# Optimization experiments

Measured on AMD Instinct MI355X. Metric: run time of the kernel, lower is better.

Reference implementation:

```python
import jax, jax.numpy as jnp
import numpy as np

BETA = 1.0 / np.sqrt(768.0).astype(np.float32)


def setup_inputs() -> dict:
    key = jax.random.key(0)
    k1, k2, k3 = jax.random.split(key, 3)
    x = jax.random.normal(k1, (32, 512, 768), dtype=jnp.float32)
    # torch nn.Linear(dim, n_prototype).weight has shape [n_prototype, dim]
    w_lookup = jax.random.normal(k2, (4096, 768), dtype=jnp.float32) * 0.02
    # torch nn.Linear(n_prototype, dim).weight has shape [dim, n_prototype]
    w_content = jax.random.normal(k3, (768, 4096), dtype=jnp.float32) * 0.02
    return {"x": x, "w_lookup": w_lookup, "w_content": w_content}


def reference(x, w_lookup, w_content):
    # scores: [b, s, n_prototype] = x @ w_lookup^T, scaled by 1/sqrt(dim)
    scores = jnp.einsum("bsd,pd->bsp", x, w_lookup) * jnp.asarray(BETA, x.dtype)
    lookup = jax.nn.softmax(scores, axis=-1)
    # content: [b, s, dim] = lookup @ w_content^T
    content = jnp.einsum("bsp,dp->bsd", lookup, w_content)
    return content  # dropout is identity in eval / p=0.0
```

## Files before the change

kernel.cpp:

```cpp
#include <hip/hip_runtime.h>
#include <hip/hip_bf16.h>


#define NTOK   16384
#define DIM    768
#define NPROT  4096
#define BETA_F 0.03608439182428583f

typedef __bf16 bf16_t;
typedef __bf16 bf16x8 __attribute__((ext_vector_type(8)));
typedef float  floatx4 __attribute__((ext_vector_type(4)));

__device__ __forceinline__ void async_copy16(const bf16_t* g, void* l) {
  __builtin_amdgcn_global_load_lds(
      (__attribute__((address_space(1))) const void*)g,
      (__attribute__((address_space(3))) void*)l, 16, 0, 0);
}

__global__ __launch_bounds__(256) void cvt_all(
    const float* __restrict__ x, const float* __restrict__ wl,
    const float* __restrict__ wc, bf16_t* __restrict__ xb,
    bf16_t* __restrict__ wlb, bf16_t* __restrict__ wcb,
    int nx8, int nw8, int nc8) {
  int i = blockIdx.x * 256 + threadIdx.x;
  const float* in; bf16_t* out; int k; int dv;
  if (i < nx8) {
    in = x; out = xb; k = i;
    const int m = k / 96, kv = k % 96;
    const int kt = kv >> 3, kr = kv & 7;
    const int sf = (((m >> 4) & 15) << 1) + (kr >> 2);
    const int l  = (m & 15) + ((kr & 3) << 4);
    dv = (((m >> 8) * 12 + kt) * 32 + sf) * 64 + l;
  } else if (i < nx8 + nw8) {
    in = wl; out = wlb; k = i - nx8;
    const int p = k / 96, kv = k % 96;
    const int kt = kv >> 3, kr = kv & 7;
    const int sf = (((p >> 4) & 15) << 1) + (kr >> 2);
    const int l  = (p & 15) + ((kr & 3) << 4);
    dv = (((p >> 8) * 12 + kt) * 32 + sf) * 64 + l;
  } else if (i < nx8 + nw8 + nc8) {
    in = wc; out = wcb; k = i - nx8 - nw8;
    const int d = k / 512, pv = k % 512;
    const int kt = pv >> 3, kr = pv & 7;
    const int dd = d % 192;
    const int sf = ((dd >> 4) << 1) + (kr >> 2);
    const int l  = (dd & 15) + ((kr & 3) << 4);
    dv = (((d / 192) * 64 + kt) * 24 + sf) * 64 + l;
  } else return;
  const float4* in4 = (const float4*)in;
  float4 a = in4[2 * k], b = in4[2 * k + 1];
  bf16x8 o;
  o[0] = (bf16_t)a.x; o[1] = (bf16_t)a.y; o[2] = (bf16_t)a.z; o[3] = (bf16_t)a.w;
  o[4] = (bf16_t)b.x; o[5] = (bf16_t)b.y; o[6] = (bf16_t)b.z; o[7] = (bf16_t)b.w;
  ((bf16x8*)out)[dv] = o;
}

__global__ __launch_bounds__(512, 2)
void gemm256(const bf16_t* __restrict__ A, const bf16_t* __restrict__ B,
             bf16_t* __restrict__ P, float* __restrict__ rowsum,
             const int K, const int N, const int nN) {
  __shared__ char lds[131072];

  const int tid = threadIdx.x;
  const int l   = tid & 63;
  const int w   = tid >> 6;
  const int wr  = w >> 2;
  const int wc  = w & 3;
  const int lr  = l & 15;

  const int nwg   = gridDim.x;
  const int chunk = nwg >> 3;
  const int wg    = (blockIdx.x & 7) * chunk + (blockIdx.x >> 3);
  const int m0    = (wg / nN) * 256;
  const int n0    = (wg % nN) * 256;

  const int T = K >> 6;
  const int abase = (m0 >> 8) * T * 16384 + l * 8;
  const int bbase = (n0 >> 8) * T * 16384 + l * 8;
  int asf[2][2], bsf[2][2];
#pragma unroll
  for (int h = 0; h < 2; ++h)
#pragma unroll
    for (int j = 0; j < 2; ++j) {
      const int s = j * 8 + w;
      asf[h][j] = ((h * 8 + (s >> 1)) * 2 + (s & 1)) * 512;
      bsf[h][j] = asf[h][j];
    }

  auto stageA = [&](int slot, int kt, int h) {
#pragma unroll
    for (int j = 0; j < 2; ++j) {
      const int s  = j * 8 + w;
      const int sf = (h * 8 + (s >> 1)) * 2 + (s & 1);
      async_copy16(A + abase + kt * 16384 + asf[h][j],
                   lds + slot * 65536 + sf * 1024);
    }
  };
  auto stageB = [&](int slot, int kt, int h) {
#pragma unroll
    for (int j = 0; j < 2; ++j) {
      const int s  = j * 8 + w;
      const int sf = (h * 8 + (s >> 1)) * 2 + (s & 1);
      async_copy16(B + bbase + kt * 16384 + bsf[h][j],
                   lds + slot * 65536 + 32768 + sf * 1024);
    }
  };

  bf16x8 af[4][2], bg[4][2];
  auto loadA = [&](int slot, int mh) {
#pragma unroll
    for (int q = 0; q < 4; ++q)
#pragma unroll
      for (int ks = 0; ks < 2; ++ks)
        af[q][ks] = *(const bf16x8*)(lds + slot * 65536 +
                        ((mh * 8 + q * 2 + wr) * 2 + ks) * 1024 + l * 16);
  };
  auto loadB = [&](int slot, int nh, int qb) {
#pragma unroll
    for (int q = 0; q < 2; ++q)
#pragma unroll
      for (int ks = 0; ks < 2; ++ks)
        bg[qb + q][ks] = *(const bf16x8*)(lds + slot * 65536 + 32768 +
                        ((nh * 8 + q * 4 + wc) * 2 + ks) * 1024 + l * 16);
  };

  const floatx4 z = {0.f, 0.f, 0.f, 0.f};
  floatx4 acc[8][4];
#pragma unroll
  for (int mt = 0; mt < 8; ++mt)
#pragma unroll
    for (int nt = 0; nt < 4; ++nt) acc[mt][nt] = z;

  auto mma = [&](int mq, int nq) {
    __builtin_amdgcn_s_setprio(1);
#pragma unroll
    for (int q = 0; q < 4; ++q)
#pragma unroll
      for (int r = 0; r < 2; ++r)
#pragma unroll
        for (int ks = 0; ks < 2; ++ks)
          acc[mq * 4 + q][nq * 2 + r] = __builtin_amdgcn_mfma_f32_16x16x32_bf16(
              af[q][ks], bg[nq * 2 + r][ks], acc[mq * 4 + q][nq * 2 + r], 0, 0, 0);
    __builtin_amdgcn_s_setprio(0);
  };

#define BAR()    __builtin_amdgcn_s_barrier()
#define LGKM0()  asm volatile("s_waitcnt lgkmcnt(0)")
#define LGKM8()  asm volatile("s_waitcnt lgkmcnt(8)")
#define VM(n)    asm volatile("s_waitcnt vmcnt(" #n ")" ::: "memory")

  stageA(0, 0, 0); stageB(0, 0, 0); stageB(0, 0, 1); stageA(0, 0, 1);
  stageA(1, 1, 0); stageB(1, 1, 0); stageB(1, 1, 1);
  VM(6);
  BAR();

#pragma unroll 1
  for (int t = 0; t < T - 2; t += 2) {
    loadA(0, 0); loadB(0, 0, 0);
    stageA(1, t + 1, 1);
    LGKM8();
    BAR(); LGKM0(); mma(0, 0); BAR();
    loadB(0, 1, 2);
    stageA(0, t + 2, 0);
    BAR(); LGKM0(); mma(0, 1); BAR();
    loadA(0, 1);
    stageB(0, t + 2, 0);
    BAR(); LGKM0(); mma(1, 1); BAR();
    stageB(0, t + 2, 1);
    BAR(); mma(1, 0); VM(6); BAR();
    loadA(1, 0); loadB(1, 0, 0);
    stageA(0, t + 2, 1);
    LGKM8();
    BAR(); LGKM0(); mma(0, 0); BAR();
    loadB(1, 1, 2);
    stageA(1, t + 3, 0);
    BAR(); LGKM0(); mma(0, 1); BAR();
    loadA(1, 1);
    stageB(1, t + 3, 0);
    BAR(); LGKM0(); mma(1, 1); BAR();
    stageB(1, t + 3, 1);
    BAR(); mma(1, 0); VM(6); BAR();
  }

  loadA(0, 0); loadB(0, 0, 0);
  stageA(1, T - 1, 1);
  LGKM8();
  BAR(); LGKM0(); mma(0, 0); BAR();
  loadB(0, 1, 2);
  BAR(); LGKM0(); mma(0, 1); BAR();
  loadA(0, 1);
  BAR(); LGKM0(); mma(1, 1); BAR();
  BAR(); mma(1, 0); VM(0); BAR();
  loadA(1, 0); loadB(1, 0, 0);
  BAR(); LGKM0(); mma(0, 0); BAR();
  loadB(1, 1, 2);
  BAR(); LGKM0(); mma(0, 1); BAR();
  loadA(1, 1);
  BAR(); LGKM0(); mma(1, 1); BAR();
  mma(1, 0);

  const int hi4 = (l >> 4) << 2;
#pragma unroll
  for (int mt = 0; mt < 8; ++mt) {
    const int row = m0 + (mt * 2 + wr) * 16 + hi4;
    float rs[4] = {0.f, 0.f, 0.f, 0.f};
#pragma unroll
    for (int nt = 0; nt < 4; ++nt) {
      const int col = n0 + (nt * 4 + wc) * 16 + lr;
#pragma unroll
      for (int i = 0; i < 4; ++i) {
        const float e = __expf(acc[mt][nt][i] * BETA_F);
        P[(row + i) * N + col] = (bf16_t)e;
        rs[i] += e;
      }
    }
#pragma unroll
    for (int i = 0; i < 4; ++i) {
      float s = rs[i];
      s += __shfl_xor(s, 1);
      s += __shfl_xor(s, 2);
      s += __shfl_xor(s, 4);
      s += __shfl_xor(s, 8);
      if (lr == 0) atomicAdd(&rowsum[row + i], s);
    }
  }
}

__global__ __launch_bounds__(512, 2)
void gemm192(const bf16_t* __restrict__ A, const bf16_t* __restrict__ B,
             float* __restrict__ O, const float* __restrict__ rowsum,
             const int K, const int N) {
  __shared__ char lds[114688];

  const int tid = threadIdx.x;
  const int l   = tid & 63;
  const int w   = tid >> 6;
  const int wr  = w >> 2;
  const int wc  = w & 3;
  const int lr  = l & 15;
  const int lk  = (l >> 4) << 3;

  const int wg = (blockIdx.x & 7) * 32 + (blockIdx.x >> 3);
  const int m0 = (wg >> 2) * 256;
  const int n0 = (wg & 3) * 192;

  int aoff[2][2];
#pragma unroll
  for (int h = 0; h < 2; ++h)
#pragma unroll
    for (int j = 0; j < 2; ++j) {
      const int s     = j * 8 + w;
      const int mfrag = h * 8 + (s >> 1);
      const int ks    = s & 1;
      aoff[h][j] = (m0 + mfrag * 16 + lr) * K + ks * 32 + lk;
    }
  const int bb = (n0 / 192) * 64 * 12288 + l * 8;
  int bsf[3];
#pragma unroll
  for (int t = 0; t < 3; ++t) bsf[t] = (t * 8 + w) * 512;

  auto stageA = [&](int slot, int kt, int h) {
#pragma unroll
    for (int j = 0; j < 2; ++j) {
      const int s  = j * 8 + w;
      const int sf = (h * 8 + (s >> 1)) * 2 + (s & 1);
      async_copy16(A + aoff[h][j] + kt * 64, lds + slot * 57344 + sf * 1024);
    }
  };
  auto stageBt = [&](int slot, int kt, int t) {
    async_copy16(B + bb + kt * 12288 + bsf[t],
                 lds + slot * 57344 + 32768 + (t * 8 + w) * 1024 + l * 16);
  };

  bf16x8 af[4][2], bg[3][2];
  auto loadA = [&](int slot, int mh) {
#pragma unroll
    for (int q = 0; q < 4; ++q)
#pragma unroll
      for (int ks = 0; ks < 2; ++ks)
        af[q][ks] = *(const bf16x8*)(lds + slot * 57344 +
                        ((mh * 8 + q * 2 + wr) * 2 + ks) * 1024 + l * 16);
  };
  auto loadBn = [&](int slot, int nlo, int ncnt) {
    for (int r = 0; r < ncnt; ++r)
#pragma unroll
      for (int ks = 0; ks < 2; ++ks)
        bg[nlo + r][ks] = *(const bf16x8*)(lds + slot * 57344 + 32768 +
                        (((wc * 3 + nlo + r) * 2 + ks) << 10) + l * 16);
  };

  const floatx4 z = {0.f, 0.f, 0.f, 0.f};
  floatx4 acc[8][3];
#pragma unroll
  for (int mt = 0; mt < 8; ++mt)
#pragma unroll
    for (int nt = 0; nt < 3; ++nt) acc[mt][nt] = z;

  auto mma = [&](int mq, int nlo, int ncnt) {
    __builtin_amdgcn_s_setprio(1);
#pragma unroll
    for (int q = 0; q < 4; ++q)
      for (int r = 0; r < ncnt; ++r)
#pragma unroll
        for (int ks = 0; ks < 2; ++ks)
          acc[mq * 4 + q][nlo + r] = __builtin_amdgcn_mfma_f32_16x16x32_bf16(
              af[q][ks], bg[nlo + r][ks], acc[mq * 4 + q][nlo + r], 0, 0, 0);
    __builtin_amdgcn_s_setprio(0);
  };

  const int T = K >> 6;

  stageA(0, 0, 0); stageA(0, 0, 1);
  stageBt(0, 0, 0); stageBt(0, 0, 1); stageBt(0, 0, 2);
  stageA(1, 1, 0);
  stageBt(1, 1, 0); stageBt(1, 1, 1); stageBt(1, 1, 2);
  VM(5);
  BAR();

#pragma unroll 1
  for (int t = 0; t < T - 2; t += 2) {
#pragma unroll
    for (int u = 0; u < 2; ++u) {
      const int p = u;
      loadA(p, 0); loadBn(p, 0, 2);
      stageA(p ^ 1, t + u + 1, 1);
      LGKM8();
      BAR(); LGKM0(); mma(0, 0, 2); BAR();
      loadBn(p, 2, 1);
      stageA(p, t + u + 2, 0);
      BAR(); LGKM0(); mma(0, 2, 1); BAR();
      loadA(p, 1);
      stageBt(p, t + u + 2, 0); stageBt(p, t + u + 2, 1);
      BAR(); LGKM0(); mma(1, 0, 2); BAR();
      stageBt(p, t + u + 2, 2);
      BAR(); mma(1, 2, 1); VM(5); BAR();
    }
  }

  loadA(0, 0); loadBn(0, 0, 2);
  stageA(1, T - 1, 1);
  LGKM8();
  BAR(); LGKM0(); mma(0, 0, 2); BAR();
  loadBn(0, 2, 1);
  BAR(); LGKM0(); mma(0, 2, 1); BAR();
  loadA(0, 1);
  BAR(); LGKM0(); mma(1, 0, 2); BAR();
  BAR(); mma(1, 2, 1); VM(0); BAR();
  loadA(1, 0); loadBn(1, 0, 2);
  BAR(); LGKM0(); mma(0, 0, 2); BAR();
  loadBn(1, 2, 1);
  BAR(); LGKM0(); mma(0, 2, 1); BAR();
  loadA(1, 1);
  BAR(); LGKM0(); mma(1, 0, 2); BAR();
  mma(1, 2, 1);

#undef BAR
#undef LGKM0
#undef LGKM8
#undef VM

  const int hi4 = (l >> 4) << 2;
#pragma unroll
  for (int mt = 0; mt < 8; ++mt) {
    const int row = m0 + (mt * 2 + wr) * 16 + hi4;
#pragma unroll
    for (int i = 0; i < 4; ++i) {
      const float inv = 1.0f / rowsum[row + i];
#pragma unroll
      for (int nt = 0; nt < 3; ++nt)
        O[(row + i) * N + n0 + (wc * 3 + nt) * 16 + lr] = acc[mt][nt][i] * inv;
    }
  }
}

__global__ __launch_bounds__(256) void hopfield_fallback(
    const float* __restrict__ x, const float* __restrict__ wl,
    const float* __restrict__ wc, float* __restrict__ out) {
  __shared__ float  xs[8 * 768];
  __shared__ bf16_t ps[8 * 4096];
  __shared__ float  rs[8];
  const int tid = threadIdx.x;
  const int r0  = blockIdx.x * 8;
  if (tid < 8) rs[tid] = 0.f;
  for (int i = tid; i < 8 * 768; i += 256)
    xs[i] = x[(r0 + (i / 768)) * 768 + (i % 768)];
  __syncthreads();

  float lsum[8] = {0, 0, 0, 0, 0, 0, 0, 0};
  for (int p = tid; p < 4096; p += 256) {
    float s[8] = {0, 0, 0, 0, 0, 0, 0, 0};
    for (int d = 0; d < 768; ++d) {
      const float wv = wl[p * 768 + d];
#pragma unroll
      for (int r = 0; r < 8; ++r) s[r] += xs[r * 768 + d] * wv;
    }
#pragma unroll
    for (int r = 0; r < 8; ++r) {
      const float e = __expf(s[r] * BETA_F);
      ps[r * 4096 + p] = (bf16_t)e;
      lsum[r] += e;
    }
  }
#pragma unroll
  for (int r = 0; r < 8; ++r) atomicAdd(&rs[r], lsum[r]);
  __syncthreads();

  for (int d = tid; d < 768; d += 256) {
    float o[8] = {0, 0, 0, 0, 0, 0, 0, 0};
    for (int p = 0; p < 4096; ++p) {
      const float wv = wc[d * 4096 + p];
#pragma unroll
      for (int r = 0; r < 8; ++r) o[r] += (float)ps[r * 4096 + p] * wv;
    }
#pragma unroll
    for (int r = 0; r < 8; ++r) out[(r0 + r) * 768 + d] = o[r] / rs[r];
  }
}

extern "C" void kernel_launch(void* const* d_in, const int* in_sizes, int n_in,
                              void* d_out, int out_size, void* d_ws, size_t ws_size,
                              hipStream_t stream) {
  (void)in_sizes; (void)n_in; (void)out_size;
  const float* x  = (const float*)d_in[0];
  const float* wl = (const float*)d_in[1];
  const float* wc = (const float*)d_in[2];
  float* out = (float*)d_out;

  const size_t xb_e = (size_t)NTOK * DIM;
  const size_t wl_e = (size_t)NPROT * DIM;
  const size_t wc_e = (size_t)DIM * NPROT;
  const size_t P_e  = (size_t)NTOK * NPROT;
  const size_t need = (xb_e + wl_e + wc_e + P_e) * 2 + (size_t)NTOK * 4;

  if (ws_size >= need) {
    char* ws = (char*)d_ws;
    bf16_t* xb  = (bf16_t*)ws;  ws += xb_e * 2;
    bf16_t* wlb = (bf16_t*)ws;  ws += wl_e * 2;
    bf16_t* wcb = (bf16_t*)ws;  ws += wc_e * 2;
    bf16_t* P   = (bf16_t*)ws;  ws += P_e * 2;
    float* rowsum = (float*)ws;

    hipMemsetAsync(rowsum, 0, NTOK * sizeof(float), stream);
    const int nx8 = (int)(xb_e / 8), nw8 = (int)(wl_e / 8), nc8 = (int)(wc_e / 8);
    cvt_all<<<(nx8 + nw8 + nc8 + 255) / 256, 256, 0, stream>>>(
        x, wl, wc, xb, wlb, wcb, nx8, nw8, nc8);
    gemm256<<<dim3((NTOK / 256) * (NPROT / 256)), 512, 0, stream>>>(
        xb, wlb, P, rowsum, DIM, NPROT, NPROT / 256);
    gemm192<<<dim3(256), 512, 0, stream>>>(
        P, wcb, out, rowsum, NPROT, DIM);
  } else {
    hopfield_fallback<<<NTOK / 8, 256, 0, stream>>>(x, wl, wc, out);
  }
}
```

Baseline: 385.8 us.

## Write softmax numerators in pre-tiled fragment layout for the second GEMM

The first GEMM's epilogue now stores exp(scores) into P in the same blocked 64-wide k-tile/fragment layout that the A operand staging uses. The second GEMM then loads A with contiguous 1KB fragment copies instead of strided row-major addressing. The aim is more coalesced, contiguous async global-to-LDS loads in the second GEMM. The cost is scattered 2-byte stores in the first kernel's epilogue and some macro redefinition shuffling.

```diff
diff --git a/kernel.cpp b/kernel.cpp
--- a/kernel.cpp
+++ b/kernel.cpp
@@ -77,14 +77,13 @@
   const int T = K >> 6;
   const int abase = (m0 >> 8) * T * 16384 + l * 8;
   const int bbase = (n0 >> 8) * T * 16384 + l * 8;
-  int asf[2][2], bsf[2][2];
+  int asf[2][2];
 #pragma unroll
   for (int h = 0; h < 2; ++h)
 #pragma unroll
     for (int j = 0; j < 2; ++j) {
       const int s = j * 8 + w;
       asf[h][j] = ((h * 8 + (s >> 1)) * 2 + (s & 1)) * 512;
-      bsf[h][j] = asf[h][j];
     }
 
   auto stageA = [&](int slot, int kt, int h) {
@@ -101,7 +100,7 @@
     for (int j = 0; j < 2; ++j) {
       const int s  = j * 8 + w;
       const int sf = (h * 8 + (s >> 1)) * 2 + (s & 1);
-      async_copy16(B + bbase + kt * 16384 + bsf[h][j],
+      async_copy16(B + bbase + kt * 16384 + asf[h][j],
                    lds + slot * 65536 + 32768 + sf * 1024);
     }
   };
@@ -199,18 +198,30 @@
   BAR(); LGKM0(); mma(1, 1); BAR();
   mma(1, 0);
 
+#undef BAR
+#undef LGKM0
+#undef LGKM8
+#undef VM
+
   const int hi4 = (l >> 4) << 2;
+  const int pband = (m0 >> 8) * 64;
 #pragma unroll
   for (int mt = 0; mt < 8; ++mt) {
-    const int row = m0 + (mt * 2 + wr) * 16 + hi4;
+    const int mfrag = mt * 2 + wr;
+    const int rowb  = m0 + mfrag * 16 + hi4;
     float rs[4] = {0.f, 0.f, 0.f, 0.f};
 #pragma unroll
     for (int nt = 0; nt < 4; ++nt) {
-      const int col = n0 + (nt * 4 + wc) * 16 + lr;
+      const int nn   = nt * 4 + wc;
+      const int kt   = (n0 >> 6) + (nn >> 2);
+      const int sf   = mfrag * 2 + ((nn >> 1) & 1);
+      const int ksel = ((nn & 1) << 1) + (lr >> 3);
+      bf16_t* dst = P + ((size_t)((pband + kt) * 32 + sf) * 512 +
+                         (hi4 + (ksel << 4)) * 8 + (lr & 7));
 #pragma unroll
       for (int i = 0; i < 4; ++i) {
         const float e = __expf(acc[mt][nt][i] * BETA_F);
-        P[(row + i) * N + col] = (bf16_t)e;
+        dst[i * 8] = (bf16_t)e;
         rs[i] += e;
       }
     }
@@ -221,7 +232,7 @@
       s += __shfl_xor(s, 2);
       s += __shfl_xor(s, 4);
       s += __shfl_xor(s, 8);
-      if (lr == 0) atomicAdd(&rowsum[row + i], s);
+      if (lr == 0) atomicAdd(&rowsum[rowb + i], s);
     }
   }
 }
@@ -238,21 +249,19 @@
   const int wr  = w >> 2;
   const int wc  = w & 3;
   const int lr  = l & 15;
-  const int lk  = (l >> 4) << 3;
 
   const int wg = (blockIdx.x & 7) * 32 + (blockIdx.x >> 3);
   const int m0 = (wg >> 2) * 256;
   const int n0 = (wg & 3) * 192;
 
-  int aoff[2][2];
+  const int abase = (m0 >> 8) * 64 * 16384 + l * 8;
+  int asf[2][2];
 #pragma unroll
   for (int h = 0; h < 2; ++h)
 #pragma unroll
     for (int j = 0; j < 2; ++j) {
-      const int s     = j * 8 + w;
-      const int mfrag = h * 8 + (s >> 1);
-      const int ks    = s & 1;
-      aoff[h][j] = (m0 + mfrag * 16 + lr) * K + ks * 32 + lk;
+      const int s = j * 8 + w;
+      asf[h][j] = ((h * 8 + (s >> 1)) * 2 + (s & 1)) * 512;
     }
   const int bb = (n0 / 192) * 64 * 12288 + l * 8;
   int bsf[3];
@@ -264,7 +273,8 @@
     for (int j = 0; j < 2; ++j) {
       const int s  = j * 8 + w;
       const int sf = (h * 8 + (s >> 1)) * 2 + (s & 1);
-      async_copy16(A + aoff[h][j] + kt * 64, lds + slot * 57344 + sf * 1024);
+      async_copy16(A + abase + kt * 16384 + asf[h][j],
+                   lds + slot * 57344 + sf * 1024);
     }
   };
   auto stageBt = [&](int slot, int kt, int t) {
@@ -307,6 +317,11 @@
               af[q][ks], bg[nlo + r][ks], acc[mq * 4 + q][nlo + r], 0, 0, 0);
     __builtin_amdgcn_s_setprio(0);
   };
+
+#define BAR()    __builtin_amdgcn_s_barrier()
+#define LGKM0()  asm volatile("s_waitcnt lgkmcnt(0)")
+#define LGKM8()  asm volatile("s_waitcnt lgkmcnt(8)")
+#define VM(n)    asm volatile("s_waitcnt vmcnt(" #n ")" ::: "memory")
 
   const int T = K >> 6;
 
```

Result: no change. 392.6 us (+1.7%).
